# Kernel tuning notes

Hardware: AMD Instinct MI355X
Metric: run time of the kernel (lower is better)

## Reference

```python
import jax, jax.numpy as jnp
import numpy as np

N = 50000        # nodes
E = 800000       # edges (avg degree 16)
F = 64           # node_feature
H = 128          # dim_h
C = 10           # num_classes
G = 512          # graphs in batch
BN_EPS = 1e-5


def setup_inputs() -> dict:
    key = jax.random.key(0)
    ks = iter(jax.random.split(key, 40))
    inp = {}
    inp['x'] = jax.random.normal(next(ks), (N, F), dtype=jnp.float32)
    inp['edge_index'] = jax.random.randint(next(ks), (2, E), 0, N, dtype=jnp.int32)
    inp['batch'] = jnp.sort(jax.random.randint(next(ks), (N,), 0, G, dtype=jnp.int32))
    # GINConv MLP params (Linear, BatchNorm1d(eval), ReLU, Linear, ReLU) x3
    in_dims = [F, H, H]
    for i in range(1, 4):
        d_in = in_dims[i - 1]
        inp[f'c{i}_w1'] = jax.random.normal(next(ks), (d_in, H), dtype=jnp.float32) * 0.05
        inp[f'c{i}_b1'] = jnp.zeros((H,), dtype=jnp.float32)
        inp[f'c{i}_g'] = jnp.ones((H,), dtype=jnp.float32)
        inp[f'c{i}_be'] = jnp.zeros((H,), dtype=jnp.float32)
        inp[f'c{i}_m'] = jax.random.normal(next(ks), (H,), dtype=jnp.float32) * 0.01
        inp[f'c{i}_v'] = jax.random.uniform(next(ks), (H,), dtype=jnp.float32) + 0.5
        inp[f'c{i}_w2'] = jax.random.normal(next(ks), (H, H), dtype=jnp.float32) * 0.05
        inp[f'c{i}_b2'] = jnp.zeros((H,), dtype=jnp.float32)
    inp['lin1_w'] = jax.random.normal(next(ks), (3 * H, 3 * H), dtype=jnp.float32) * 0.05
    inp['lin1_b'] = jnp.zeros((3 * H,), dtype=jnp.float32)
    inp['lin2_w'] = jax.random.normal(next(ks), (3 * H, C), dtype=jnp.float32) * 0.05
    inp['lin2_b'] = jnp.zeros((C,), dtype=jnp.float32)
    return inp


def _mlp(h, w1, b1, g, be, m, v, w2, b2):
    h = h @ w1 + b1
    h = (h - m) * jax.lax.rsqrt(v + BN_EPS) * g + be  # BatchNorm1d (eval)
    h = jax.nn.relu(h)
    return jax.nn.relu(h @ w2 + b2)


def _gin_conv(x, src, dst, w1, b1, g, be, m, v, w2, b2):
    # GINConv, eps=0: MLP(x_i + sum_{j->i} x_j)
    agg = jax.ops.segment_sum(x[src], dst, num_segments=N)
    return _mlp(x + agg, w1, b1, g, be, m, v, w2, b2)


def reference(x, edge_index, batch,
              c1_w1, c1_b1, c1_g, c1_be, c1_m, c1_v, c1_w2, c1_b2,
              c2_w1, c2_b1, c2_g, c2_be, c2_m, c2_v, c2_w2, c2_b2,
              c3_w1, c3_b1, c3_g, c3_be, c3_m, c3_v, c3_w2, c3_b2,
              lin1_w, lin1_b, lin2_w, lin2_b):
    src, dst = edge_index[0], edge_index[1]
    h1 = _gin_conv(x, src, dst, c1_w1, c1_b1, c1_g, c1_be, c1_m, c1_v, c1_w2, c1_b2)
    h2 = _gin_conv(h1, src, dst, c2_w1, c2_b1, c2_g, c2_be, c2_m, c2_v, c2_w2, c2_b2)
    h3 = _gin_conv(h2, src, dst, c3_w1, c3_b1, c3_g, c3_be, c3_m, c3_v, c3_w2, c3_b2)
    p1 = jax.ops.segment_sum(h1, batch, num_segments=G)  # global_add_pool
    p2 = jax.ops.segment_sum(h2, batch, num_segments=G)
    p3 = jax.ops.segment_sum(h3, batch, num_segments=G)
    h = jnp.concatenate((p1, p2, p3), axis=1)  # [G, 3H]
    h = jax.nn.relu(h @ lin1_w + lin1_b)
    # dropout is identity in eval mode
    h = h @ lin2_w + lin2_b
    return jax.nn.log_softmax(h, axis=1)
```

## Files before the change

### kernel.cpp

```cpp
#include <hip/hip_runtime.h>
#include <math.h>
#include <stdint.h>

static constexpr int NN = 50000;
static constexpr int NE = 800000;
static constexpr int NG = 512;
static constexpr int NB = (NN + 255) / 256;
static constexpr float BNEPS = 1e-5f;

typedef __bf16 bf16x8 __attribute__((ext_vector_type(8)));
typedef __bf16 bf16x2 __attribute__((ext_vector_type(2)));
typedef float f32x4 __attribute__((ext_vector_type(4)));

__device__ __forceinline__ uint32_t pack_bf16(float x, float y) {
    bf16x2 v; v[0] = (__bf16)x; v[1] = (__bf16)y;
    return __builtin_bit_cast(uint32_t, v);
}
__device__ __forceinline__ float2 unpack_bf16(uint32_t u) {
    bf16x2 v = __builtin_bit_cast(bf16x2, u);
    return make_float2((float)v[0], (float)v[1]);
}


__global__ void degree_kernel(const int* __restrict__ dst, int* __restrict__ deg,
                              int* __restrict__ rank) {
    int e = blockIdx.x * blockDim.x + threadIdx.x;
    if (e < NE) rank[e] = atomicAdd(&deg[dst[e]], 1);
}

__global__ __launch_bounds__(256) void blocksum_kernel(const int* __restrict__ deg,
                                                       int* __restrict__ bsum) {
    int i = blockIdx.x * 256 + threadIdx.x;
    int v = (i < NN) ? deg[i] : 0;
#pragma unroll
    for (int off = 32; off; off >>= 1) v += __shfl_down(v, off, 64);
    __shared__ int s[4];
    if ((threadIdx.x & 63) == 0) s[threadIdx.x >> 6] = v;
    __syncthreads();
    if (threadIdx.x == 0) bsum[blockIdx.x] = s[0] + s[1] + s[2] + s[3];
}

__global__ __launch_bounds__(256) void scanb_kernel(const int* __restrict__ bsum,
                                                    int* __restrict__ bscan,
                                                    int* __restrict__ row_ptr) {
    __shared__ int s[256];
    int t = threadIdx.x;
    int v = (t < NB) ? bsum[t] : 0;
    s[t] = v;
    __syncthreads();
    for (int off = 1; off < 256; off <<= 1) {
        int u = (t >= off) ? s[t - off] : 0;
        __syncthreads();
        s[t] += u;
        __syncthreads();
    }
    if (t < NB) bscan[t] = s[t] - v;
    if (t == NB - 1) row_ptr[NN] = s[t];
}

__global__ __launch_bounds__(256) void scanfinal_kernel(const int* __restrict__ deg,
                                                        const int* __restrict__ bscan,
                                                        int* __restrict__ row_ptr) {
    __shared__ int s[256];
    int t = threadIdx.x;
    int i = blockIdx.x * 256 + t;
    int v = (i < NN) ? deg[i] : 0;
    s[t] = v;
    __syncthreads();
    for (int off = 1; off < 256; off <<= 1) {
        int u = (t >= off) ? s[t - off] : 0;
        __syncthreads();
        s[t] += u;
        __syncthreads();
    }
    if (i < NN) row_ptr[i] = bscan[blockIdx.x] + s[t] - v;
}

__global__ void fill_kernel(const int* __restrict__ src, const int* __restrict__ dst,
                            const int* __restrict__ row_ptr, const int* __restrict__ rank,
                            int* __restrict__ cols) {
    int e = blockIdx.x * blockDim.x + threadIdx.x;
    if (e < NE) cols[row_ptr[dst[e]] + rank[e]] = src[e];
}


__global__ void convert_x_kernel(const float* __restrict__ x, __bf16* __restrict__ xb) {
    int i = blockIdx.x * blockDim.x + threadIdx.x;
    if (i < NN * 16) {
        float4 v = *(const float4*)&x[i * 4];
        xb[i * 4 + 0] = (__bf16)v.x;
        xb[i * 4 + 1] = (__bf16)v.y;
        xb[i * 4 + 2] = (__bf16)v.z;
        xb[i * 4 + 3] = (__bf16)v.w;
    }
}

__global__ void prep_w_kernel(const float* s0, const float* s1, const float* s2,
                              const float* s3, const float* s4, const float* s5,
                              const float* s6,
                              __bf16* d0, __bf16* d1, __bf16* d2,
                              __bf16* d3, __bf16* d4, __bf16* d5, __bf16* d6) {
    int i = blockIdx.x * blockDim.x + threadIdx.x;
    if (i < 8192) {
        int l = i;           int n = l / 64,  k = l % 64;  d0[l] = (__bf16)s0[k * 128 + n];
    } else if (i < 24576) {
        int l = i - 8192;    int n = l / 128, k = l % 128; d1[l] = (__bf16)s1[k * 128 + n];
    } else if (i < 40960) {
        int l = i - 24576;   int n = l / 128, k = l % 128; d2[l] = (__bf16)s2[k * 128 + n];
    } else if (i < 57344) {
        int l = i - 40960;   int n = l / 128, k = l % 128; d3[l] = (__bf16)s3[k * 128 + n];
    } else if (i < 73728) {
        int l = i - 57344;   int n = l / 128, k = l % 128; d4[l] = (__bf16)s4[k * 128 + n];
    } else if (i < 90112) {
        int l = i - 73728;   int n = l / 128, k = l % 128; d5[l] = (__bf16)s5[k * 128 + n];
    } else if (i < 237568) {
        int l = i - 90112;   int n = l / 384, k = l % 384; d6[l] = (__bf16)s6[k * 384 + n];
    }
}


__global__ void gather64_kernel(const __bf16* __restrict__ in, const int* __restrict__ row_ptr,
                                const int* __restrict__ cols, __bf16* __restrict__ agg) {
    int node = blockIdx.x * (blockDim.x >> 6) + (threadIdx.x >> 6);
    int lane = threadIdx.x & 63;
    if (node >= NN) return;
    int beg = row_ptr[node], end = row_ptr[node + 1];
    float acc = (float)in[(size_t)node * 64 + lane];
    int i = beg;
    for (; i + 4 <= end; i += 4) {
        int c0 = cols[i], c1 = cols[i + 1], c2 = cols[i + 2], c3 = cols[i + 3];
        float v0 = (float)in[(size_t)c0 * 64 + lane];
        float v1 = (float)in[(size_t)c1 * 64 + lane];
        float v2 = (float)in[(size_t)c2 * 64 + lane];
        float v3 = (float)in[(size_t)c3 * 64 + lane];
        acc += (v0 + v1) + (v2 + v3);
    }
    for (; i < end; ++i) acc += (float)in[(size_t)cols[i] * 64 + lane];
    agg[(size_t)node * 64 + lane] = (__bf16)acc;
}

__global__ void gather128_kernel(const __bf16* __restrict__ in, const int* __restrict__ row_ptr,
                                 const int* __restrict__ cols, __bf16* __restrict__ agg) {
    int node = blockIdx.x * (blockDim.x >> 6) + (threadIdx.x >> 6);
    int lane = threadIdx.x & 63;
    if (node >= NN) return;
    const uint32_t* inu = (const uint32_t*)in;
    uint32_t* aggu = (uint32_t*)agg;
    int beg = row_ptr[node], end = row_ptr[node + 1];
    float2 acc = unpack_bf16(inu[(size_t)node * 64 + lane]);
    int i = beg;
    for (; i + 4 <= end; i += 4) {
        int c0 = cols[i], c1 = cols[i + 1], c2 = cols[i + 2], c3 = cols[i + 3];
        uint32_t u0 = inu[(size_t)c0 * 64 + lane];
        uint32_t u1 = inu[(size_t)c1 * 64 + lane];
        uint32_t u2 = inu[(size_t)c2 * 64 + lane];
        uint32_t u3 = inu[(size_t)c3 * 64 + lane];
        float2 v0 = unpack_bf16(u0), v1 = unpack_bf16(u1);
        float2 v2 = unpack_bf16(u2), v3 = unpack_bf16(u3);
        acc.x += (v0.x + v1.x) + (v2.x + v3.x);
        acc.y += (v0.y + v1.y) + (v2.y + v3.y);
    }
    for (; i < end; ++i) {
        float2 v = unpack_bf16(inu[(size_t)cols[i] * 64 + lane]);
        acc.x += v.x; acc.y += v.y;
    }
    aggu[(size_t)node * 64 + lane] = pack_bf16(acc.x, acc.y);
}


template <int K, bool WOUT>
__global__ __launch_bounds__(512, 1) void mlp_mfma_kernel(
    const __bf16* __restrict__ agg,
    const __bf16* __restrict__ w1t,
    const float* __restrict__ b1,
    const float* __restrict__ g, const float* __restrict__ be,
    const float* __restrict__ m, const float* __restrict__ v,
    const __bf16* __restrict__ w2t,
    const float* __restrict__ b2,
    __bf16* __restrict__ out,
    const int* __restrict__ batch,
    float* __restrict__ p,
    int col_off)
{
    constexpr int KP = K + 8;
    constexpr int KP2 = 136;
    __shared__ alignas(16) __bf16 sA[64 * KP];
    __shared__ alignas(16) __bf16 sW1[128 * KP];
    __shared__ alignas(16) __bf16 sW2[128 * KP2];
    __shared__ alignas(16) __bf16 sT[64 * KP2];
    __shared__ alignas(16) __bf16 sOut[64 * KP2];
    __shared__ int sBatch[64];

    int tid = threadIdx.x;
    int wid = tid >> 6, lane = tid & 63;
    int wr = wid >> 1, wc = wid & 1;
    int l15 = lane & 15, lq = lane >> 4;
    int rowbase = blockIdx.x * 64;

    for (int idx = tid; idx < 64 * (K / 8); idx += 512) {
        int r = idx / (K / 8), kc = idx % (K / 8);
        int n = rowbase + r;
        uint4 val = make_uint4(0, 0, 0, 0);
        if (n < NN) val = *(const uint4*)&agg[(size_t)n * K + kc * 8];
        *(uint4*)&sA[r * KP + kc * 8] = val;
    }
    for (int idx = tid; idx < 128 * (K / 8); idx += 512) {
        int n = idx / (K / 8), kc = idx % (K / 8);
        *(uint4*)&sW1[n * KP + kc * 8] = *(const uint4*)&w1t[n * K + kc * 8];
    }
    for (int idx = tid; idx < 128 * 16; idx += 512) {
        int n = idx >> 4, kc = idx & 15;
        *(uint4*)&sW2[n * KP2 + kc * 8] = *(const uint4*)&w2t[n * 128 + kc * 8];
    }
    if (tid < 64) {
        int n = rowbase + tid;
        sBatch[tid] = (n < NN) ? batch[n] : -1;
    }
    __syncthreads();

    f32x4 acc[4] = {};
#pragma unroll
    for (int ks = 0; ks < K / 32; ++ks) {
        bf16x8 a = *(const bf16x8*)&sA[(wr * 16 + l15) * KP + ks * 32 + lq * 8];
#pragma unroll
        for (int nf = 0; nf < 4; ++nf) {
            bf16x8 b = *(const bf16x8*)&sW1[(wc * 64 + nf * 16 + l15) * KP + ks * 32 + lq * 8];
            acc[nf] = __builtin_amdgcn_mfma_f32_16x16x32_bf16(a, b, acc[nf], 0, 0, 0);
        }
    }
#pragma unroll
    for (int nf = 0; nf < 4; ++nf) {
        int c = wc * 64 + nf * 16 + l15;
        float sc = g[c] * rsqrtf(v[c] + BNEPS);
        float sh = be[c] + (b1[c] - m[c]) * sc;
#pragma unroll
        for (int r = 0; r < 4; ++r) {
            int row = wr * 16 + lq * 4 + r;
            float t = fmaxf(acc[nf][r] * sc + sh, 0.f);
            sT[row * KP2 + c] = (__bf16)t;
        }
    }
    __syncthreads();

    f32x4 acc2[4] = {};
#pragma unroll
    for (int ks = 0; ks < 4; ++ks) {
        bf16x8 a = *(const bf16x8*)&sT[(wr * 16 + l15) * KP2 + ks * 32 + lq * 8];
#pragma unroll
        for (int nf = 0; nf < 4; ++nf) {
            bf16x8 b = *(const bf16x8*)&sW2[(wc * 64 + nf * 16 + l15) * KP2 + ks * 32 + lq * 8];
            acc2[nf] = __builtin_amdgcn_mfma_f32_16x16x32_bf16(a, b, acc2[nf], 0, 0, 0);
        }
    }
#pragma unroll
    for (int nf = 0; nf < 4; ++nf) {
        int c = wc * 64 + nf * 16 + l15;
        float bb = b2[c];
#pragma unroll
        for (int r = 0; r < 4; ++r) {
            int row = wr * 16 + lq * 4 + r;
            float o = fmaxf(acc2[nf][r] + bb, 0.f);
            sOut[row * KP2 + c] = (__bf16)o;
        }
    }
    __syncthreads();

    if constexpr (WOUT) {
        for (int idx = tid; idx < 64 * 16; idx += 512) {
            int r = idx >> 4, kc = idx & 15;
            int n = rowbase + r;
            if (n < NN)
                *(uint4*)&out[(size_t)n * 128 + kc * 8] = *(const uint4*)&sOut[r * KP2 + kc * 8];
        }
    }

    {
        int f = tid & 127;
        int chunk = tid >> 7;
        float pacc = 0.f;
        int cur = -1;
#pragma unroll
        for (int i = 0; i < 16; ++i) {
            int row = chunk * 16 + i;
            int b = sBatch[row];
            if (b < 0) break;
            if (b != cur) {
                if (cur >= 0) atomicAdd(&p[cur * 384 + col_off + f], pacc);
                pacc = 0.f;
                cur = b;
            }
            pacc += (float)sOut[row * KP2 + f];
        }
        if (cur >= 0) atomicAdd(&p[cur * 384 + col_off + f], pacc);
    }
}


__global__ __launch_bounds__(512, 1) void head1_kernel(const float* __restrict__ p,
                                                       const __bf16* __restrict__ lin1t,
                                                       const float* __restrict__ b1,
                                                       float* __restrict__ hrelu) {
    constexpr int KPA = 392;
    constexpr int KPW = 136;
    __shared__ alignas(16) __bf16 sA[64 * KPA];
    __shared__ alignas(16) __bf16 sW[128 * KPW];

    int tid = threadIdx.x;
    int wid = tid >> 6, lane = tid & 63;
    int wr = wid >> 1, wc = wid & 1;
    int l15 = lane & 15, lq = lane >> 4;
    int rowbase = blockIdx.x * 64;
    int colbase = blockIdx.y * 128;

    for (int idx = tid; idx < 64 * 48; idx += 512) {
        int r = idx / 48, kc = idx % 48;
        const float* srcp = &p[(rowbase + r) * 384 + kc * 8];
        float4 v0 = *(const float4*)srcp;
        float4 v1 = *(const float4*)(srcp + 4);
        bf16x8 o;
        o[0] = (__bf16)v0.x; o[1] = (__bf16)v0.y; o[2] = (__bf16)v0.z; o[3] = (__bf16)v0.w;
        o[4] = (__bf16)v1.x; o[5] = (__bf16)v1.y; o[6] = (__bf16)v1.z; o[7] = (__bf16)v1.w;
        *(bf16x8*)&sA[r * KPA + kc * 8] = o;
    }

    f32x4 acc[4] = {};
#pragma unroll
    for (int kchunk = 0; kchunk < 3; ++kchunk) {
        for (int idx = tid; idx < 128 * 16; idx += 512) {
            int n = idx >> 4, kc = idx & 15;
            *(uint4*)&sW[n * KPW + kc * 8] =
                *(const uint4*)&lin1t[(colbase + n) * 384 + kchunk * 128 + kc * 8];
        }
        __syncthreads();
#pragma unroll
        for (int ks = 0; ks < 4; ++ks) {
            bf16x8 a = *(const bf16x8*)&sA[(wr * 16 + l15) * KPA + kchunk * 128 + ks * 32 + lq * 8];
#pragma unroll
            for (int nf = 0; nf < 4; ++nf) {
                bf16x8 b = *(const bf16x8*)&sW[(wc * 64 + nf * 16 + l15) * KPW + ks * 32 + lq * 8];
                acc[nf] = __builtin_amdgcn_mfma_f32_16x16x32_bf16(a, b, acc[nf], 0, 0, 0);
            }
        }
        __syncthreads();
    }
#pragma unroll
    for (int nf = 0; nf < 4; ++nf) {
        int col = colbase + wc * 64 + nf * 16 + l15;
        float bb = b1[col];
#pragma unroll
        for (int r = 0; r < 4; ++r) {
            int row = rowbase + wr * 16 + lq * 4 + r;
            hrelu[row * 384 + col] = fmaxf(acc[nf][r] + bb, 0.f);
        }
    }
}


__global__ __launch_bounds__(256) void head2_kernel(const float* __restrict__ hrelu,
                                                    const float* __restrict__ w2,
                                                    const float* __restrict__ b2,
                                                    float* __restrict__ out) {
    int wid = threadIdx.x >> 6, lane = threadIdx.x & 63;
    int gidx = blockIdx.x * 4 + wid;
    const float* hr = &hrelu[gidx * 384 + lane * 6];
    float h[6];
#pragma unroll
    for (int u = 0; u < 6; ++u) h[u] = hr[u];
    float logit[10];
#pragma unroll
    for (int c = 0; c < 10; ++c) {
        float s = 0.f;
#pragma unroll
        for (int u = 0; u < 6; ++u) s = fmaf(h[u], w2[(lane * 6 + u) * 10 + c], s);
#pragma unroll
        for (int off = 32; off; off >>= 1) s += __shfl_xor(s, off, 64);
        logit[c] = s + b2[c];
    }
    float mx = logit[0];
#pragma unroll
    for (int c = 1; c < 10; ++c) mx = fmaxf(mx, logit[c]);
    float se = 0.f;
#pragma unroll
    for (int c = 0; c < 10; ++c) se += expf(logit[c] - mx);
    float lse = logf(se);
    float val = 0.f;
#pragma unroll
    for (int c = 0; c < 10; ++c) if (lane == c) val = logit[c];
    if (lane < 10) out[gidx * 10 + lane] = val - mx - lse;
}


static inline char* align_up(char* ptr, size_t a) {
    return (char*)(((uintptr_t)ptr + a - 1) & ~(uintptr_t)(a - 1));
}

extern "C" void kernel_launch(void* const* d_in, const int* in_sizes, int n_in,
                              void* d_out, int out_size, void* d_ws, size_t ws_size,
                              hipStream_t stream) {
    const float* x = (const float*)d_in[0];
    const int* ei = (const int*)d_in[1];
    const int* batch = (const int*)d_in[2];
    const float* c_w1[3], *c_b1[3], *c_g[3], *c_be[3], *c_m[3], *c_v[3], *c_w2[3], *c_b2[3];
    for (int i = 0; i < 3; ++i) {
        int base = 3 + i * 8;
        c_w1[i] = (const float*)d_in[base + 0];
        c_b1[i] = (const float*)d_in[base + 1];
        c_g[i]  = (const float*)d_in[base + 2];
        c_be[i] = (const float*)d_in[base + 3];
        c_m[i]  = (const float*)d_in[base + 4];
        c_v[i]  = (const float*)d_in[base + 5];
        c_w2[i] = (const float*)d_in[base + 6];
        c_b2[i] = (const float*)d_in[base + 7];
    }
    const float* lin1_w = (const float*)d_in[27];
    const float* lin1_b = (const float*)d_in[28];
    const float* lin2_w = (const float*)d_in[29];
    const float* lin2_b = (const float*)d_in[30];
    const int* src = ei;
    const int* dst = ei + NE;
    float* out = (float*)d_out;

    char* ws = (char*)d_ws;
    __bf16* xb  = (__bf16*)ws; ws = align_up(ws + (size_t)NN * 64 * 2, 256);
    __bf16* agg = (__bf16*)ws; ws = align_up(ws + (size_t)NN * 128 * 2, 256);
    __bf16* hA  = (__bf16*)ws; ws = align_up(ws + (size_t)NN * 128 * 2, 256);
    __bf16* hB  = (__bf16*)ws; ws = align_up(ws + (size_t)NN * 128 * 2, 256);
    float* p    = (float*)ws;  ws = align_up(ws + (size_t)NG * 384 * 4, 256);
    float* hrelu = (float*)ws; ws = align_up(ws + (size_t)NG * 384 * 4, 256);
    int* csr_row = (int*)ws;   ws = align_up(ws + (size_t)(NN + 1) * 4, 256);
    int* cursor  = (int*)ws;   ws = align_up(ws + (size_t)NN * 4, 256);
    int* csr_src = (int*)ws;   ws = align_up(ws + (size_t)NE * 4, 256);
    int* rank    = (int*)ws;   ws = align_up(ws + (size_t)NE * 4, 256);
    int* bsum    = (int*)ws;   ws = align_up(ws + (size_t)NB * 4, 256);
    int* bscan   = (int*)ws;   ws = align_up(ws + (size_t)NB * 4, 256);
    __bf16* w1t[3]; __bf16* w2t[3];
    for (int i = 0; i < 3; ++i) {
        int K = (i == 0) ? 64 : 128;
        w1t[i] = (__bf16*)ws; ws = align_up(ws + (size_t)128 * K * 2, 256);
        w2t[i] = (__bf16*)ws; ws = align_up(ws + (size_t)128 * 128 * 2, 256);
    }
    __bf16* lin1t = (__bf16*)ws; ws = align_up(ws + (size_t)384 * 384 * 2, 256);

    hipMemsetAsync(cursor, 0, (size_t)NN * 4, stream);
    degree_kernel<<<(NE + 255) / 256, 256, 0, stream>>>(dst, cursor, rank);
    blocksum_kernel<<<NB, 256, 0, stream>>>(cursor, bsum);
    scanb_kernel<<<1, 256, 0, stream>>>(bsum, bscan, csr_row);
    scanfinal_kernel<<<NB, 256, 0, stream>>>(cursor, bscan, csr_row);
    fill_kernel<<<(NE + 255) / 256, 256, 0, stream>>>(src, dst, csr_row, rank, csr_src);
    hipMemsetAsync(p, 0, (size_t)NG * 384 * 4, stream);

    convert_x_kernel<<<(NN * 16 + 255) / 256, 256, 0, stream>>>(x, xb);
    prep_w_kernel<<<(237568 + 255) / 256, 256, 0, stream>>>(
        c_w1[0], c_w1[1], c_w1[2], c_w2[0], c_w2[1], c_w2[2], lin1_w,
        w1t[0], w1t[1], w1t[2], w2t[0], w2t[1], w2t[2], lin1t);

    const int GATHER_BLOCKS = (NN + 3) / 4;
    const int MLP_BLOCKS = (NN + 63) / 64;

    gather64_kernel<<<GATHER_BLOCKS, 256, 0, stream>>>(xb, csr_row, csr_src, agg);
    mlp_mfma_kernel<64, true><<<MLP_BLOCKS, 512, 0, stream>>>(agg, w1t[0], c_b1[0], c_g[0], c_be[0],
                                                              c_m[0], c_v[0], w2t[0], c_b2[0], hA,
                                                              batch, p, 0);

    gather128_kernel<<<GATHER_BLOCKS, 256, 0, stream>>>(hA, csr_row, csr_src, agg);
    mlp_mfma_kernel<128, true><<<MLP_BLOCKS, 512, 0, stream>>>(agg, w1t[1], c_b1[1], c_g[1], c_be[1],
                                                               c_m[1], c_v[1], w2t[1], c_b2[1], hB,
                                                               batch, p, 128);

    gather128_kernel<<<GATHER_BLOCKS, 256, 0, stream>>>(hB, csr_row, csr_src, agg);
    mlp_mfma_kernel<128, false><<<MLP_BLOCKS, 512, 0, stream>>>(agg, w1t[2], c_b1[2], c_g[2], c_be[2],
                                                                c_m[2], c_v[2], w2t[2], c_b2[2], nullptr,
                                                                batch, p, 256);

    head1_kernel<<<dim3(8, 3), 512, 0, stream>>>(p, lin1t, lin1_b, hrelu);
    head2_kernel<<<128, 256, 0, stream>>>(hrelu, lin2_w, lin2_b, out);
}
```

Before: 269.8 us.

## Shrink CSR indices to uint16, widen gather unroll, fuse prep kernels

Stores CSR column indices and per-edge ranks as 16-bit values, which is valid because there are 50000 nodes. This halves index traffic in CSR construction and in the three gathers. The gather kernels now unroll eight neighbours with two independent accumulators and run 512-thread blocks handling eight nodes each, to raise memory-level parallelism. The feature conversion and weight transpose kernels are merged into one launch to save launch overhead; the 16-bit indices tie the code to node counts below 65536.

```diff
diff --git a/kernel.cpp b/kernel.cpp
--- a/kernel.cpp
+++ b/kernel.cpp
@@ -23,9 +23,9 @@
 
 
 __global__ void degree_kernel(const int* __restrict__ dst, int* __restrict__ deg,
-                              int* __restrict__ rank) {
+                              uint16_t* __restrict__ rank) {
     int e = blockIdx.x * blockDim.x + threadIdx.x;
-    if (e < NE) rank[e] = atomicAdd(&deg[dst[e]], 1);
+    if (e < NE) rank[e] = (uint16_t)atomicAdd(&deg[dst[e]], 1);
 }
 
 __global__ __launch_bounds__(256) void blocksum_kernel(const int* __restrict__ deg,
@@ -77,94 +77,114 @@
 }
 
 __global__ void fill_kernel(const int* __restrict__ src, const int* __restrict__ dst,
-                            const int* __restrict__ row_ptr, const int* __restrict__ rank,
-                            int* __restrict__ cols) {
+                            const int* __restrict__ row_ptr, const uint16_t* __restrict__ rank,
+                            uint16_t* __restrict__ cols) {
     int e = blockIdx.x * blockDim.x + threadIdx.x;
-    if (e < NE) cols[row_ptr[dst[e]] + rank[e]] = src[e];
-}
-
-
-__global__ void convert_x_kernel(const float* __restrict__ x, __bf16* __restrict__ xb) {
+    if (e < NE) cols[row_ptr[dst[e]] + (int)rank[e]] = (uint16_t)src[e];
+}
+
+
+__global__ void prep_kernel(const float* __restrict__ x, __bf16* __restrict__ xb,
+                            const float* s0, const float* s1, const float* s2,
+                            const float* s3, const float* s4, const float* s5,
+                            const float* s6,
+                            __bf16* d0, __bf16* d1, __bf16* d2,
+                            __bf16* d3, __bf16* d4, __bf16* d5, __bf16* d6) {
     int i = blockIdx.x * blockDim.x + threadIdx.x;
-    if (i < NN * 16) {
+    if (i < 800000) {
         float4 v = *(const float4*)&x[i * 4];
         xb[i * 4 + 0] = (__bf16)v.x;
         xb[i * 4 + 1] = (__bf16)v.y;
         xb[i * 4 + 2] = (__bf16)v.z;
         xb[i * 4 + 3] = (__bf16)v.w;
-    }
-}
-
-__global__ void prep_w_kernel(const float* s0, const float* s1, const float* s2,
-                              const float* s3, const float* s4, const float* s5,
-                              const float* s6,
-                              __bf16* d0, __bf16* d1, __bf16* d2,
-                              __bf16* d3, __bf16* d4, __bf16* d5, __bf16* d6) {
-    int i = blockIdx.x * blockDim.x + threadIdx.x;
-    if (i < 8192) {
-        int l = i;           int n = l / 64,  k = l % 64;  d0[l] = (__bf16)s0[k * 128 + n];
-    } else if (i < 24576) {
-        int l = i - 8192;    int n = l / 128, k = l % 128; d1[l] = (__bf16)s1[k * 128 + n];
-    } else if (i < 40960) {
-        int l = i - 24576;   int n = l / 128, k = l % 128; d2[l] = (__bf16)s2[k * 128 + n];
-    } else if (i < 57344) {
-        int l = i - 40960;   int n = l / 128, k = l % 128; d3[l] = (__bf16)s3[k * 128 + n];
-    } else if (i < 73728) {
-        int l = i - 57344;   int n = l / 128, k = l % 128; d4[l] = (__bf16)s4[k * 128 + n];
-    } else if (i < 90112) {
-        int l = i - 73728;   int n = l / 128, k = l % 128; d5[l] = (__bf16)s5[k * 128 + n];
-    } else if (i < 237568) {
-        int l = i - 90112;   int n = l / 384, k = l % 384; d6[l] = (__bf16)s6[k * 384 + n];
-    }
-}
-
-
-__global__ void gather64_kernel(const __bf16* __restrict__ in, const int* __restrict__ row_ptr,
-                                const int* __restrict__ cols, __bf16* __restrict__ agg) {
-    int node = blockIdx.x * (blockDim.x >> 6) + (threadIdx.x >> 6);
+        return;
+    }
+    int j = i - 800000;
+    if (j < 8192) {
+        int l = j;           int n = l / 64,  k = l % 64;  d0[l] = (__bf16)s0[k * 128 + n];
+    } else if (j < 24576) {
+        int l = j - 8192;    int n = l / 128, k = l % 128; d1[l] = (__bf16)s1[k * 128 + n];
+    } else if (j < 40960) {
+        int l = j - 24576;   int n = l / 128, k = l % 128; d2[l] = (__bf16)s2[k * 128 + n];
+    } else if (j < 57344) {
+        int l = j - 40960;   int n = l / 128, k = l % 128; d3[l] = (__bf16)s3[k * 128 + n];
+    } else if (j < 73728) {
+        int l = j - 57344;   int n = l / 128, k = l % 128; d4[l] = (__bf16)s4[k * 128 + n];
+    } else if (j < 90112) {
+        int l = j - 73728;   int n = l / 128, k = l % 128; d5[l] = (__bf16)s5[k * 128 + n];
+    } else if (j < 237568) {
+        int l = j - 90112;   int n = l / 384, k = l % 384; d6[l] = (__bf16)s6[k * 384 + n];
+    }
+}
+
+
+__global__ __launch_bounds__(512) void gather64_kernel(const __bf16* __restrict__ in,
+                                                       const int* __restrict__ row_ptr,
+                                                       const uint16_t* __restrict__ cols,
+                                                       __bf16* __restrict__ agg) {
+    int node = blockIdx.x * 8 + (threadIdx.x >> 6);
     int lane = threadIdx.x & 63;
     if (node >= NN) return;
     int beg = row_ptr[node], end = row_ptr[node + 1];
-    float acc = (float)in[(size_t)node * 64 + lane];
+    float acc0 = (float)in[(size_t)node * 64 + lane];
+    float acc1 = 0.f;
     int i = beg;
-    for (; i + 4 <= end; i += 4) {
+    for (; i + 8 <= end; i += 8) {
         int c0 = cols[i], c1 = cols[i + 1], c2 = cols[i + 2], c3 = cols[i + 3];
+        int c4 = cols[i + 4], c5 = cols[i + 5], c6 = cols[i + 6], c7 = cols[i + 7];
         float v0 = (float)in[(size_t)c0 * 64 + lane];
         float v1 = (float)in[(size_t)c1 * 64 + lane];
         float v2 = (float)in[(size_t)c2 * 64 + lane];
         float v3 = (float)in[(size_t)c3 * 64 + lane];
-        acc += (v0 + v1) + (v2 + v3);
-    }
-    for (; i < end; ++i) acc += (float)in[(size_t)cols[i] * 64 + lane];
-    agg[(size_t)node * 64 + lane] = (__bf16)acc;
-}
-
-__global__ void gather128_kernel(const __bf16* __restrict__ in, const int* __restrict__ row_ptr,
-                                 const int* __restrict__ cols, __bf16* __restrict__ agg) {
-    int node = blockIdx.x * (blockDim.x >> 6) + (threadIdx.x >> 6);
+        float v4 = (float)in[(size_t)c4 * 64 + lane];
+        float v5 = (float)in[(size_t)c5 * 64 + lane];
+        float v6 = (float)in[(size_t)c6 * 64 + lane];
+        float v7 = (float)in[(size_t)c7 * 64 + lane];
+        acc0 += (v0 + v1) + (v2 + v3);
+        acc1 += (v4 + v5) + (v6 + v7);
+    }
+    for (; i < end; ++i) acc0 += (float)in[(size_t)cols[i] * 64 + lane];
+    agg[(size_t)node * 64 + lane] = (__bf16)(acc0 + acc1);
+}
+
+__global__ __launch_bounds__(512) void gather128_kernel(const __bf16* __restrict__ in,
+                                                        const int* __restrict__ row_ptr,
+                                                        const uint16_t* __restrict__ cols,
+                                                        __bf16* __restrict__ agg) {
+    int node = blockIdx.x * 8 + (threadIdx.x >> 6);
     int lane = threadIdx.x & 63;
     if (node >= NN) return;
     const uint32_t* inu = (const uint32_t*)in;
     uint32_t* aggu = (uint32_t*)agg;
     int beg = row_ptr[node], end = row_ptr[node + 1];
-    float2 acc = unpack_bf16(inu[(size_t)node * 64 + lane]);
+    float2 a0 = unpack_bf16(inu[(size_t)node * 64 + lane]);
+    float2 a1 = make_float2(0.f, 0.f);
     int i = beg;
-    for (; i + 4 <= end; i += 4) {
+    for (; i + 8 <= end; i += 8) {
         int c0 = cols[i], c1 = cols[i + 1], c2 = cols[i + 2], c3 = cols[i + 3];
+        int c4 = cols[i + 4], c5 = cols[i + 5], c6 = cols[i + 6], c7 = cols[i + 7];
         uint32_t u0 = inu[(size_t)c0 * 64 + lane];
         uint32_t u1 = inu[(size_t)c1 * 64 + lane];
         uint32_t u2 = inu[(size_t)c2 * 64 + lane];
         uint32_t u3 = inu[(size_t)c3 * 64 + lane];
+        uint32_t u4 = inu[(size_t)c4 * 64 + lane];
+        uint32_t u5 = inu[(size_t)c5 * 64 + lane];
+        uint32_t u6 = inu[(size_t)c6 * 64 + lane];
+        uint32_t u7 = inu[(size_t)c7 * 64 + lane];
         float2 v0 = unpack_bf16(u0), v1 = unpack_bf16(u1);
         float2 v2 = unpack_bf16(u2), v3 = unpack_bf16(u3);
-        acc.x += (v0.x + v1.x) + (v2.x + v3.x);
-        acc.y += (v0.y + v1.y) + (v2.y + v3.y);
+        float2 v4 = unpack_bf16(u4), v5 = unpack_bf16(u5);
+        float2 v6 = unpack_bf16(u6), v7 = unpack_bf16(u7);
+        a0.x += (v0.x + v1.x) + (v2.x + v3.x);
+        a0.y += (v0.y + v1.y) + (v2.y + v3.y);
+        a1.x += (v4.x + v5.x) + (v6.x + v7.x);
+        a1.y += (v4.y + v5.y) + (v6.y + v7.y);
     }
     for (; i < end; ++i) {
         float2 v = unpack_bf16(inu[(size_t)cols[i] * 64 + lane]);
-        acc.x += v.x; acc.y += v.y;
-    }
-    aggu[(size_t)node * 64 + lane] = pack_bf16(acc.x, acc.y);
+        a0.x += v.x; a0.y += v.y;
+    }
+    aggu[(size_t)node * 64 + lane] = pack_bf16(a0.x + a1.x, a0.y + a1.y);
 }
 
 
@@ -429,8 +449,8 @@
     float* hrelu = (float*)ws; ws = align_up(ws + (size_t)NG * 384 * 4, 256);
     int* csr_row = (int*)ws;   ws = align_up(ws + (size_t)(NN + 1) * 4, 256);
     int* cursor  = (int*)ws;   ws = align_up(ws + (size_t)NN * 4, 256);
-    int* csr_src = (int*)ws;   ws = align_up(ws + (size_t)NE * 4, 256);
-    int* rank    = (int*)ws;   ws = align_up(ws + (size_t)NE * 4, 256);
+    uint16_t* csr_src = (uint16_t*)ws; ws = align_up(ws + (size_t)NE * 2, 256);
+    uint16_t* rank    = (uint16_t*)ws; ws = align_up(ws + (size_t)NE * 2, 256);
     int* bsum    = (int*)ws;   ws = align_up(ws + (size_t)NB * 4, 256);
     int* bscan   = (int*)ws;   ws = align_up(ws + (size_t)NB * 4, 256);
     __bf16* w1t[3]; __bf16* w2t[3];
@@ -449,25 +469,25 @@
     fill_kernel<<<(NE + 255) / 256, 256, 0, stream>>>(src, dst, csr_row, rank, csr_src);
     hipMemsetAsync(p, 0, (size_t)NG * 384 * 4, stream);
 
-    convert_x_kernel<<<(NN * 16 + 255) / 256, 256, 0, stream>>>(x, xb);
-    prep_w_kernel<<<(237568 + 255) / 256, 256, 0, stream>>>(
+    prep_kernel<<<(800000 + 237568 + 255) / 256, 256, 0, stream>>>(
+        x, xb,
         c_w1[0], c_w1[1], c_w1[2], c_w2[0], c_w2[1], c_w2[2], lin1_w,
         w1t[0], w1t[1], w1t[2], w2t[0], w2t[1], w2t[2], lin1t);
 
-    const int GATHER_BLOCKS = (NN + 3) / 4;
+    const int GATHER_BLOCKS = (NN + 7) / 8;
     const int MLP_BLOCKS = (NN + 63) / 64;
 
-    gather64_kernel<<<GATHER_BLOCKS, 256, 0, stream>>>(xb, csr_row, csr_src, agg);
+    gather64_kernel<<<GATHER_BLOCKS, 512, 0, stream>>>(xb, csr_row, csr_src, agg);
     mlp_mfma_kernel<64, true><<<MLP_BLOCKS, 512, 0, stream>>>(agg, w1t[0], c_b1[0], c_g[0], c_be[0],
                                                               c_m[0], c_v[0], w2t[0], c_b2[0], hA,
                                                               batch, p, 0);
 
-    gather128_kernel<<<GATHER_BLOCKS, 256, 0, stream>>>(hA, csr_row, csr_src, agg);
+    gather128_kernel<<<GATHER_BLOCKS, 512, 0, stream>>>(hA, csr_row, csr_src, agg);
     mlp_mfma_kernel<128, true><<<MLP_BLOCKS, 512, 0, stream>>>(agg, w1t[1], c_b1[1], c_g[1], c_be[1],
                                                                c_m[1], c_v[1], w2t[1], c_b2[1], hB,
                                                                batch, p, 128);
 
-    gather128_kernel<<<GATHER_BLOCKS, 256, 0, stream>>>(hB, csr_row, csr_src, agg);
+    gather128_kernel<<<GATHER_BLOCKS, 512, 0, stream>>>(hB, csr_row, csr_src, agg);
     mlp_mfma_kernel<128, false><<<MLP_BLOCKS, 512, 0, stream>>>(agg, w1t[2], c_b1[2], c_g[2], c_be[2],
                                                                 c_m[2], c_v[2], w2t[2], c_b2[2], nullptr,
                                                                 batch, p, 256);
```

After: 273.2 us. No clear change (+1.3%).
